# Kernel tuning notes

Measured on AMD Instinct MI355X. Metric: run time of the kernel, lower is better.

The kernel has to match this reference:

```python
import jax, jax.numpy as jnp
import numpy as np

NEG_INF = -1e30


def setup_inputs() -> dict:
    key = jax.random.key(0)
    ks = jax.random.split(key, 8)
    B, N, I, O, H = 8, 1024, 64, 32, 4
    return {
        "x": jax.random.normal(ks[0], (B, N, I), dtype=jnp.float32),
        "adj": jax.random.randint(ks[1], (N, N), 0, 2, dtype=jnp.int32),
        "source_prior": jax.random.normal(ks[2], (B, N), dtype=jnp.float32),
        "beta": jax.random.normal(ks[3], (H,), dtype=jnp.float32),
        "weight": jax.random.normal(ks[4], (H, I, O), dtype=jnp.float32) * (1.0 / np.sqrt(I)),
        "attn_src": jax.random.normal(ks[5], (H, O), dtype=jnp.float32) * (1.0 / np.sqrt(O)),
        "attn_dst": jax.random.normal(ks[6], (H, O), dtype=jnp.float32) * (1.0 / np.sqrt(O)),
        "bias": jnp.zeros((H, O), dtype=jnp.float32),
    }


def reference(x, adj, source_prior, beta, weight, attn_src, attn_dst, bias):
    B, N, _ = x.shape
    H, _, O = weight.shape
    # Per-head projection + bias: [B,H,N,O]
    projected = jnp.einsum('bni,hio->bhno', x, weight) + bias[None, :, None, :]
    src_scores = jnp.einsum('bhnd,hd->bhn', projected, attn_src)  # [B,H,N]
    dst_scores = jnp.einsum('bhnd,hd->bhn', projected, attn_dst)  # [B,H,N]
    # Additive attention logits: [B,H,dst,src]
    logits = jax.nn.leaky_relu(dst_scores[..., :, None] + src_scores[..., None, :],
                               negative_slope=0.2)
    # Source-prior correction
    gain = jax.nn.softplus(beta).reshape(1, H, 1, 1)
    logits = logits + gain * source_prior[:, None, None, :]
    # Masked softmax over sources; fully-masked rows stay zero
    mask = (adj != 0)[None, None, :, :]  # [1,1,N,N]
    masked = jnp.where(mask, logits, NEG_INF)
    row_max = jnp.max(masked, axis=-1, keepdims=True)
    row_max = jnp.where(jnp.isfinite(row_max) & (row_max > NEG_INF / 2),
                        row_max, jnp.zeros_like(row_max))
    exp_logits = jnp.where(mask, jnp.exp(logits - row_max), 0.0)
    eps = jnp.finfo(logits.dtype).eps
    denom = jnp.maximum(jnp.sum(exp_logits, axis=-1, keepdims=True), eps)
    attention = exp_logits / denom  # [B,H,N,N]
    # Weighted aggregation: [B,H,N,O]
    output = jnp.einsum('bhij,bhjd->bhid', attention, projected)
    # concat=True: [B,N,H*O]
    encoded = jnp.transpose(output, (0, 2, 1, 3)).reshape(B, N, H * O)
    return encoded
```

## Files before the change

kernel.cpp:

```cpp
#include <hip/hip_runtime.h>
#include <math.h>

#define NB 8
#define NN 1024
#define NI 64
#define NO 32
#define NH 4
#define LOG2E 1.4426950408889634f

typedef _Float16 half8 __attribute__((ext_vector_type(8)));
typedef _Float16 half2v __attribute__((ext_vector_type(2)));
typedef float floatx4 __attribute__((ext_vector_type(4)));

__global__ __launch_bounds__(256) void k_proj(
    const float* __restrict__ x, const int* __restrict__ adj,
    const float* __restrict__ prior, const float* __restrict__ beta,
    const float* __restrict__ weight, const float* __restrict__ attn_src,
    const float* __restrict__ attn_dst, const float* __restrict__ bias,
    _Float16* __restrict__ projT,
    float* __restrict__ src_s, float* __restrict__ dst_s, float* __restrict__ gp_,
    unsigned char* __restrict__ adjb)
{
    __shared__ __align__(16) float xs[32 * 64];
    __shared__ __align__(16) float ws[4 * 64 * 36];
    const int t = threadIdx.x;
    const int ntile = blockIdx.x, b = blockIdx.y;
    const int n0b = ntile * 32;
    #pragma unroll
    for (int k = 0; k < 4; ++k) {
        const int g = (b * 32 + ntile) * 1024 + k * 256 + t;
        const int4 v = ((const int4*)adj)[g];
        ((unsigned int*)adjb)[g] =
            (v.x ? 1u : 0u) | ((v.y ? 1u : 0u) << 8) |
            ((v.z ? 1u : 0u) << 16) | ((v.w ? 1u : 0u) << 24);
    }
    {
        const float4* xsrc = (const float4*)(x + ((size_t)b * NN + n0b) * NI);
        float4* xd = (float4*)xs;
        xd[t] = xsrc[t];
        xd[t + 256] = xsrc[t + 256];
    }
    #pragma unroll
    for (int k = 0; k < 8; ++k) {
        const int e = t + k * 256;
        const int h = e >> 9, rem = e & 511, i = rem >> 3, o4 = rem & 7;
        *(float4*)&ws[h * 2304 + i * 36 + o4 * 4] =
            *(const float4*)(weight + (h * NI + i) * NO + o4 * 4);
    }
    __syncthreads();

    const int o4 = t & 7, h = (t >> 3) & 3, ng = t >> 5;
    const int o0 = o4 * 4, nl0 = ng * 4;
    float acc[4][4];
    #pragma unroll
    for (int kn = 0; kn < 4; ++kn)
        #pragma unroll
        for (int oo = 0; oo < 4; ++oo) acc[kn][oo] = 0.f;

    #pragma unroll 4
    for (int i = 0; i < NI; ++i) {
        const float4 wv = *(const float4*)&ws[h * 2304 + i * 36 + o0];
        #pragma unroll
        for (int kn = 0; kn < 4; ++kn) {
            const float xv = xs[(nl0 + kn) * 64 + i];
            acc[kn][0] = fmaf(xv, wv.x, acc[kn][0]);
            acc[kn][1] = fmaf(xv, wv.y, acc[kn][1]);
            acc[kn][2] = fmaf(xv, wv.z, acc[kn][2]);
            acc[kn][3] = fmaf(xv, wv.w, acc[kn][3]);
        }
    }
    const float4 bv  = *(const float4*)(bias + h * NO + o0);
    const float4 asv = *(const float4*)(attn_src + h * NO + o0);
    const float4 adv = *(const float4*)(attn_dst + h * NO + o0);
    const int bh = b * NH + h;
    float ssum[4], dsum[4];
    #pragma unroll
    for (int kn = 0; kn < 4; ++kn) {
        acc[kn][0] += bv.x; acc[kn][1] += bv.y;
        acc[kn][2] += bv.z; acc[kn][3] += bv.w;
        ssum[kn] = acc[kn][0]*asv.x + acc[kn][1]*asv.y + acc[kn][2]*asv.z + acc[kn][3]*asv.w;
        dsum[kn] = acc[kn][0]*adv.x + acc[kn][1]*adv.y + acc[kn][2]*adv.z + acc[kn][3]*adv.w;
    }
    #pragma unroll
    for (int oo = 0; oo < 4; ++oo) {
        half2v h0, h1;
        h0[0] = (_Float16)acc[0][oo]; h0[1] = (_Float16)acc[1][oo];
        h1[0] = (_Float16)acc[2][oo]; h1[1] = (_Float16)acc[3][oo];
        _Float16* pp = projT + ((size_t)(bh * NO + o0 + oo)) * NN + n0b + nl0;
        *(half2v*)pp = h0;
        *(half2v*)(pp + 2) = h1;
    }
    #pragma unroll
    for (int msk = 1; msk <= 4; msk <<= 1) {
        #pragma unroll
        for (int kn = 0; kn < 4; ++kn) {
            ssum[kn] += __shfl_xor(ssum[kn], msk, 64);
            dsum[kn] += __shfl_xor(dsum[kn], msk, 64);
        }
    }
    if (o4 == 0) {
        const float bx = beta[h];
        const float sp = fmaxf(bx, 0.f) + log1pf(__expf(-fabsf(bx)));
        #pragma unroll
        for (int kn = 0; kn < 4; ++kn) {
            const int n = n0b + nl0 + kn;
            src_s[bh * NN + n] = LOG2E * ssum[kn];
            dst_s[bh * NN + n] = LOG2E * dsum[kn];
            gp_[bh * NN + n]   = LOG2E * sp * prior[b * NN + n];
        }
    }
}

__global__ __launch_bounds__(256, 4) void k_attn(
    const unsigned char* __restrict__ adjb,
    const _Float16* __restrict__ projT,
    const float* __restrict__ src_s, const float* __restrict__ dst_s,
    const float* __restrict__ gp_,
    float* __restrict__ out)
{
    __shared__ __align__(16) float srcs[NN];
    __shared__ __align__(16) float gps[NN];
    __shared__ float red[8];
    __shared__ float part[4][16][33];
    __shared__ float ps[4][16];

    const int t = threadIdx.x;
    const int lane = t & 63, wave = t >> 6;
    const int rowtile = blockIdx.x, h = blockIdx.y, b = blockIdx.z;
    const int bh = b * NH + h;

    const float4 s4 = ((const float4*)(src_s + bh * NN))[t];
    const float4 g4 = ((const float4*)(gp_ + bh * NN))[t];
    ((float4*)srcs)[t] = s4;
    ((float4*)gps)[t]  = g4;
    float s_l = fmaxf(fmaxf(s4.x, s4.y), fmaxf(s4.z, s4.w));
    float g_l = fmaxf(fmaxf(g4.x, g4.y), fmaxf(g4.z, g4.w));
    #pragma unroll
    for (int msk = 1; msk <= 32; msk <<= 1) {
        s_l = fmaxf(s_l, __shfl_xor(s_l, msk, 64));
        g_l = fmaxf(g_l, __shfl_xor(g_l, msk, 64));
    }
    if (lane == 0) { red[wave * 2] = s_l; red[wave * 2 + 1] = g_l; }
    __syncthreads();
    const float S = fmaxf(fmaxf(red[0], red[2]), fmaxf(red[4], red[6]));
    const float G = fmaxf(fmaxf(red[1], red[3]), fmaxf(red[5], red[7]));

    const int m = lane & 15, quad = lane >> 4;
    const int d = rowtile * 16 + m;
    const float dregl = dst_s[bh * NN + d];
    const float rmcl = fmaxf(dregl + S, 0.f) + G;
    const unsigned char* adjr = adjb + (size_t)d * NN;
    const _Float16* ptr0 = projT + (size_t)(bh * NO + m) * NN;
    const _Float16* ptr1 = ptr0 + 16 * NN;

    floatx4 acc0 = {0.f, 0.f, 0.f, 0.f}, acc1 = {0.f, 0.f, 0.f, 0.f};
    float psum = 0.f;
    int sg = wave * 256 + quad * 8;
    uint2  aa  = *(const uint2*)(adjr + sg);
    half8  vb0 = *(const half8*)(ptr0 + sg);
    half8  vb1 = *(const half8*)(ptr1 + sg);

    #pragma unroll
    for (int st = 0; st < 8; ++st) {
        const uint2 ac = aa;
        const half8 b0 = vb0, b1 = vb1;
        const int sgc = sg;
        if (st < 7) {
            sg += 32;
            aa  = *(const uint2*)(adjr + sg);
            vb0 = *(const half8*)(ptr0 + sg);
            vb1 = *(const half8*)(ptr1 + sg);
        }
        float sv[8], gv[8];
        *(float4*)&sv[0] = *(const float4*)&srcs[sgc];
        *(float4*)&sv[4] = *(const float4*)&srcs[sgc + 4];
        *(float4*)&gv[0] = *(const float4*)&gps[sgc];
        *(float4*)&gv[4] = *(const float4*)&gps[sgc + 4];
        float p[8];
        #pragma unroll
        for (int j = 0; j < 8; ++j) {
            const unsigned int bit =
                ((j < 4 ? (ac.x >> (8 * j)) : (ac.y >> (8 * (j - 4)))) & 1u);
            const float ts = dregl + sv[j];
            const float lk = fmaxf(ts, 0.2f * ts);
            const float arg = bit ? (lk + gv[j] - rmcl) : -1e30f;
            p[j] = exp2f(arg);
            psum += p[j];
        }
        half8 af;
        #pragma unroll
        for (int j = 0; j < 8; ++j) af[j] = (_Float16)p[j];
        acc0 = __builtin_amdgcn_mfma_f32_16x16x32_f16(af, b0, acc0, 0, 0, 0);
        acc1 = __builtin_amdgcn_mfma_f32_16x16x32_f16(af, b1, acc1, 0, 0, 0);
    }
    psum += __shfl_xor(psum, 16, 64);
    psum += __shfl_xor(psum, 32, 64);

    #pragma unroll
    for (int r = 0; r < 4; ++r) {
        part[wave][quad * 4 + r][m]      = acc0[r];
        part[wave][quad * 4 + r][16 + m] = acc1[r];
    }
    if (quad == 0) ps[wave][m] = psum;
    __syncthreads();

    const int row = t >> 4, col = t & 15;
    const float denom = ps[0][row] + ps[1][row] + ps[2][row] + ps[3][row];
    const float inv = 1.f / fmaxf(denom, 1.1920929e-07f);
    const float v0 = part[0][row][col] + part[1][row][col] +
                     part[2][row][col] + part[3][row][col];
    const float v1 = part[0][row][16 + col] + part[1][row][16 + col] +
                     part[2][row][16 + col] + part[3][row][16 + col];
    float* go = out + ((size_t)(b * NN + rowtile * 16 + row)) * (NH * NO) + h * NO;
    go[col]      = v0 * inv;
    go[16 + col] = v1 * inv;
}

extern "C" void kernel_launch(void* const* d_in, const int* in_sizes, int n_in,
                              void* d_out, int out_size, void* d_ws, size_t ws_size,
                              hipStream_t stream) {
    (void)in_sizes; (void)n_in; (void)out_size; (void)ws_size;
    const float* x        = (const float*)d_in[0];
    const int*   adj      = (const int*)d_in[1];
    const float* prior    = (const float*)d_in[2];
    const float* beta     = (const float*)d_in[3];
    const float* weight   = (const float*)d_in[4];
    const float* attn_src = (const float*)d_in[5];
    const float* attn_dst = (const float*)d_in[6];
    const float* bias     = (const float*)d_in[7];
    float* out = (float*)d_out;

    _Float16* projT = (_Float16*)d_ws;
    float* src_s = (float*)((char*)d_ws + (1 << 21));
    float* dst_s = src_s + NB * NH * NN;
    float* gpb   = dst_s + NB * NH * NN;
    unsigned char* adjb = (unsigned char*)(gpb + NB * NH * NN);

    hipLaunchKernelGGL(k_proj, dim3(32, 8), dim3(256), 0, stream,
                       x, adj, prior, beta, weight, attn_src, attn_dst, bias,
                       projT, src_s, dst_s, gpb, adjb);
    hipLaunchKernelGGL(k_attn, dim3(64, 4, 8), dim3(256), 0, stream,
                       adjb, projT, src_s, dst_s, gpb, out);
}
```

Before: 104.8 us.

## Process 32 destination rows per block in attention kernel, reusing projT loads

The attention kernel now covers 32 destination rows per block instead of 16, so each loaded projT fragment feeds four MFMAs instead of two, and the grid halves to 1024 blocks. Row sums move from shuffle reductions onto MFMAs against a ones vector. The leaky-relu is rewritten as a max of two precomputed affine forms using a prescaled 0.2*src array in LDS, and the block index is remapped so blocks with the same rowtile run close together and share adjacency rows in cache. Output writes become float4 stores, and k_proj writes half4 instead of two half2. The cost is more registers and LDS per block, fewer blocks, and two extra MFMAs per step.

```diff
diff --git a/kernel.cpp b/kernel.cpp
--- a/kernel.cpp
+++ b/kernel.cpp
@@ -9,7 +9,7 @@
 #define LOG2E 1.4426950408889634f
 
 typedef _Float16 half8 __attribute__((ext_vector_type(8)));
-typedef _Float16 half2v __attribute__((ext_vector_type(2)));
+typedef _Float16 half4v __attribute__((ext_vector_type(4)));
 typedef float floatx4 __attribute__((ext_vector_type(4)));
 
 __global__ __launch_bounds__(256) void k_proj(
@@ -83,12 +83,10 @@
     }
     #pragma unroll
     for (int oo = 0; oo < 4; ++oo) {
-        half2v h0, h1;
-        h0[0] = (_Float16)acc[0][oo]; h0[1] = (_Float16)acc[1][oo];
-        h1[0] = (_Float16)acc[2][oo]; h1[1] = (_Float16)acc[3][oo];
-        _Float16* pp = projT + ((size_t)(bh * NO + o0 + oo)) * NN + n0b + nl0;
-        *(half2v*)pp = h0;
-        *(half2v*)(pp + 2) = h1;
+        half4v hv;
+        hv[0] = (_Float16)acc[0][oo]; hv[1] = (_Float16)acc[1][oo];
+        hv[2] = (_Float16)acc[2][oo]; hv[3] = (_Float16)acc[3][oo];
+        *(half4v*)(projT + ((size_t)(bh * NO + o0 + oo)) * NN + n0b + nl0) = hv;
     }
     #pragma unroll
     for (int msk = 1; msk <= 4; msk <<= 1) {
@@ -119,20 +117,26 @@
     float* __restrict__ out)
 {
     __shared__ __align__(16) float srcs[NN];
+    __shared__ __align__(16) float srcs2[NN];
     __shared__ __align__(16) float gps[NN];
     __shared__ float red[8];
-    __shared__ float part[4][16][33];
-    __shared__ float ps[4][16];
+    __shared__ float part[4][32][33];
+    __shared__ float ps[4][32];
 
     const int t = threadIdx.x;
     const int lane = t & 63, wave = t >> 6;
-    const int rowtile = blockIdx.x, h = blockIdx.y, b = blockIdx.z;
+    const int blk = blockIdx.x;
+    const int rowtile = blk >> 5, h = (blk >> 3) & 3, b = blk & 7;
     const int bh = b * NH + h;
+    const int d0 = rowtile * 32;
 
     const float4 s4 = ((const float4*)(src_s + bh * NN))[t];
     const float4 g4 = ((const float4*)(gp_ + bh * NN))[t];
     ((float4*)srcs)[t] = s4;
-    ((float4*)gps)[t]  = g4;
+    float4 s42; s42.x = 0.2f * s4.x; s42.y = 0.2f * s4.y;
+    s42.z = 0.2f * s4.z; s42.w = 0.2f * s4.w;
+    ((float4*)srcs2)[t] = s42;
+    ((float4*)gps)[t] = g4;
     float s_l = fmaxf(fmaxf(s4.x, s4.y), fmaxf(s4.z, s4.w));
     float g_l = fmaxf(fmaxf(g4.x, g4.y), fmaxf(g4.z, g4.w));
     #pragma unroll
@@ -146,74 +150,99 @@
     const float G = fmaxf(fmaxf(red[1], red[3]), fmaxf(red[5], red[7]));
 
     const int m = lane & 15, quad = lane >> 4;
-    const int d = rowtile * 16 + m;
-    const float dregl = dst_s[bh * NN + d];
-    const float rmcl = fmaxf(dregl + S, 0.f) + G;
-    const unsigned char* adjr = adjb + (size_t)d * NN;
+    const int dlo = d0 + m, dhi = d0 + 16 + m;
+    const float drl = dst_s[bh * NN + dlo];
+    const float drh = dst_s[bh * NN + dhi];
+    const float Rlo = fmaxf(drl + S, 0.f) + G;
+    const float Rhi = fmaxf(drh + S, 0.f) + G;
+    const float c1l = drl - Rlo, c2l = 0.2f * drl - Rlo;
+    const float c1h = drh - Rhi, c2h = 0.2f * drh - Rhi;
+    const unsigned char* arl = adjb + (size_t)dlo * NN;
+    const unsigned char* arh = adjb + (size_t)dhi * NN;
     const _Float16* ptr0 = projT + (size_t)(bh * NO + m) * NN;
     const _Float16* ptr1 = ptr0 + 16 * NN;
 
-    floatx4 acc0 = {0.f, 0.f, 0.f, 0.f}, acc1 = {0.f, 0.f, 0.f, 0.f};
-    float psum = 0.f;
+    half8 onesv;
+    #pragma unroll
+    for (int j = 0; j < 8; ++j) onesv[j] = (_Float16)1.0f;
+
+    floatx4 aLL = {0,0,0,0}, aLH = {0,0,0,0}, aHL = {0,0,0,0}, aHH = {0,0,0,0};
+    floatx4 pL = {0,0,0,0}, pH = {0,0,0,0};
+
     int sg = wave * 256 + quad * 8;
-    uint2  aa  = *(const uint2*)(adjr + sg);
-    half8  vb0 = *(const half8*)(ptr0 + sg);
-    half8  vb1 = *(const half8*)(ptr1 + sg);
+    uint2 al = *(const uint2*)(arl + sg);
+    uint2 ah = *(const uint2*)(arh + sg);
+    half8 vb0 = *(const half8*)(ptr0 + sg);
+    half8 vb1 = *(const half8*)(ptr1 + sg);
 
     #pragma unroll
     for (int st = 0; st < 8; ++st) {
-        const uint2 ac = aa;
+        const uint2 acl = al, ach = ah;
         const half8 b0 = vb0, b1 = vb1;
         const int sgc = sg;
         if (st < 7) {
             sg += 32;
-            aa  = *(const uint2*)(adjr + sg);
+            al = *(const uint2*)(arl + sg);
+            ah = *(const uint2*)(arh + sg);
             vb0 = *(const half8*)(ptr0 + sg);
             vb1 = *(const half8*)(ptr1 + sg);
         }
-        float sv[8], gv[8];
+        float sv[8], s2[8], gv[8];
         *(float4*)&sv[0] = *(const float4*)&srcs[sgc];
         *(float4*)&sv[4] = *(const float4*)&srcs[sgc + 4];
+        *(float4*)&s2[0] = *(const float4*)&srcs2[sgc];
+        *(float4*)&s2[4] = *(const float4*)&srcs2[sgc + 4];
         *(float4*)&gv[0] = *(const float4*)&gps[sgc];
         *(float4*)&gv[4] = *(const float4*)&gps[sgc + 4];
-        float p[8];
+        half8 afl, afh;
         #pragma unroll
         for (int j = 0; j < 8; ++j) {
-            const unsigned int bit =
-                ((j < 4 ? (ac.x >> (8 * j)) : (ac.y >> (8 * (j - 4)))) & 1u);
-            const float ts = dregl + sv[j];
-            const float lk = fmaxf(ts, 0.2f * ts);
-            const float arg = bit ? (lk + gv[j] - rmcl) : -1e30f;
-            p[j] = exp2f(arg);
-            psum += p[j];
-        }
-        half8 af;
-        #pragma unroll
-        for (int j = 0; j < 8; ++j) af[j] = (_Float16)p[j];
-        acc0 = __builtin_amdgcn_mfma_f32_16x16x32_f16(af, b0, acc0, 0, 0, 0);
-        acc1 = __builtin_amdgcn_mfma_f32_16x16x32_f16(af, b1, acc1, 0, 0, 0);
-    }
-    psum += __shfl_xor(psum, 16, 64);
-    psum += __shfl_xor(psum, 32, 64);
+            const unsigned int bl_ =
+                ((j < 4 ? (acl.x >> (8 * j)) : (acl.y >> (8 * (j - 4)))) & 1u);
+            const unsigned int bh_ =
+                ((j < 4 ? (ach.x >> (8 * j)) : (ach.y >> (8 * (j - 4)))) & 1u);
+            const float argl = fmaxf(sv[j] + c1l, s2[j] + c2l) + gv[j];
+            const float argh = fmaxf(sv[j] + c1h, s2[j] + c2h) + gv[j];
+            afl[j] = (_Float16)exp2f(bl_ ? argl : -1e30f);
+            afh[j] = (_Float16)exp2f(bh_ ? argh : -1e30f);
+        }
+        aLL = __builtin_amdgcn_mfma_f32_16x16x32_f16(afl, b0, aLL, 0, 0, 0);
+        aLH = __builtin_amdgcn_mfma_f32_16x16x32_f16(afl, b1, aLH, 0, 0, 0);
+        aHL = __builtin_amdgcn_mfma_f32_16x16x32_f16(afh, b0, aHL, 0, 0, 0);
+        aHH = __builtin_amdgcn_mfma_f32_16x16x32_f16(afh, b1, aHH, 0, 0, 0);
+        pL  = __builtin_amdgcn_mfma_f32_16x16x32_f16(afl, onesv, pL, 0, 0, 0);
+        pH  = __builtin_amdgcn_mfma_f32_16x16x32_f16(afh, onesv, pH, 0, 0, 0);
+    }
 
     #pragma unroll
     for (int r = 0; r < 4; ++r) {
-        part[wave][quad * 4 + r][m]      = acc0[r];
-        part[wave][quad * 4 + r][16 + m] = acc1[r];
-    }
-    if (quad == 0) ps[wave][m] = psum;
+        const int row = quad * 4 + r;
+        part[wave][row][m]           = aLL[r];
+        part[wave][row][16 + m]      = aLH[r];
+        part[wave][16 + row][m]      = aHL[r];
+        part[wave][16 + row][16 + m] = aHH[r];
+    }
+    if (m == 0) {
+        #pragma unroll
+        for (int r = 0; r < 4; ++r) {
+            ps[wave][quad * 4 + r]      = pL[r];
+            ps[wave][16 + quad * 4 + r] = pH[r];
+        }
+    }
     __syncthreads();
 
-    const int row = t >> 4, col = t & 15;
+    const int row = t >> 3, c0 = (t & 7) * 4;
     const float denom = ps[0][row] + ps[1][row] + ps[2][row] + ps[3][row];
     const float inv = 1.f / fmaxf(denom, 1.1920929e-07f);
-    const float v0 = part[0][row][col] + part[1][row][col] +
-                     part[2][row][col] + part[3][row][col];
-    const float v1 = part[0][row][16 + col] + part[1][row][16 + col] +
-                     part[2][row][16 + col] + part[3][row][16 + col];
-    float* go = out + ((size_t)(b * NN + rowtile * 16 + row)) * (NH * NO) + h * NO;
-    go[col]      = v0 * inv;
-    go[16 + col] = v1 * inv;
+    float4 r4;
+    float* rp = &r4.x;
+    #pragma unroll
+    for (int i = 0; i < 4; ++i) {
+        const int c = c0 + i;
+        rp[i] = (part[0][row][c] + part[1][row][c] +
+                 part[2][row][c] + part[3][row][c]) * inv;
+    }
+    *(float4*)(out + ((size_t)(b * NN + d0 + row)) * (NH * NO) + h * NO + c0) = r4;
 }
 
 extern "C" void kernel_launch(void* const* d_in, const int* in_sizes, int n_in,
@@ -239,6 +268,6 @@
     hipLaunchKernelGGL(k_proj, dim3(32, 8), dim3(256), 0, stream,
                        x, adj, prior, beta, weight, attn_src, attn_dst, bias,
                        projT, src_s, dst_s, gpb, adjb);
-    hipLaunchKernelGGL(k_attn, dim3(64, 4, 8), dim3(256), 0, stream,
+    hipLaunchKernelGGL(k_attn, dim3(1024), dim3(256), 0, stream,
                        adjb, projT, src_s, dst_s, gpb, out);
 }
```

After: 96.77 us. -7.7%, faster.
